# Performance work log

Measured on AMD Instinct MI355X. Metric: run time of the kernel, lower is better.

The kernel has to match this reference:

```python
import jax, jax.numpy as jnp
import numpy as np

B, A, EMBED, HIDDEN, PROJ = 256, 16, 1024, 1024, 256


def setup_inputs() -> dict:
    key = jax.random.key(0)
    k0, k1, k2 = jax.random.split(key, 3)
    return {
        "agent_embeddings": jax.random.normal(k0, (B, A, EMBED), dtype=jnp.float32),
        "w1": jax.random.normal(k1, (EMBED, HIDDEN), dtype=jnp.float32) * (1.0 / np.sqrt(EMBED)),
        "b1": jnp.zeros((HIDDEN,), dtype=jnp.float32),
        "w2": jax.random.normal(k2, (HIDDEN, PROJ), dtype=jnp.float32) * (1.0 / np.sqrt(HIDDEN)),
        "b2": jnp.zeros((PROJ,), dtype=jnp.float32),
        "log_scale": jnp.asarray(0.0, dtype=jnp.float32),  # log(init_logit_scale=1.0)
        "logit_bias": jnp.asarray(0.0, dtype=jnp.float32),
    }


def reference(agent_embeddings, w1, b1, w2, b2, log_scale, logit_bias):
    b, a, d = agent_embeddings.shape
    n = b * a
    x = agent_embeddings.reshape(n, d)
    # MLP projector: Linear -> GELU (exact, torch default) -> [dropout=identity at eval] -> Linear
    h = jax.nn.gelu(x @ w1 + b1, approximate=False)
    p = h @ w2 + b2  # [N, proj_dim]
    z = p / jnp.linalg.norm(p, axis=-1, keepdims=True)
    # cosine similarity logits, scaled + biased
    logits = (z @ z.T) * jnp.exp(log_scale) + logit_bias  # [N, N]
    # block-diagonal labels: 1 iff same batch element
    ids = jnp.arange(n) // a
    m1 = jnp.where(ids[:, None] == ids[None, :], 1.0, -1.0)  # 2*labels - 1
    loglik = jax.nn.log_sigmoid(m1 * logits)
    loss = jnp.mean(-jnp.sum(loglik, axis=-1))
    embeddings = z.reshape(b, a, -1)
    return embeddings, loss, logits
```

## Files before the change

### kernel.cpp

```cpp
#include <hip/hip_runtime.h>
#include <math.h>


#define NTOK 4096
#define DEMB 1024
#define DHID 1024
#define DPRJ 256

typedef __attribute__((ext_vector_type(8))) short bf16x8;
typedef __attribute__((ext_vector_type(4))) float f32x4;

typedef __attribute__((address_space(3))) void lds_void_t;
typedef __attribute__((address_space(1))) const void gbl_void_t;

static __device__ __forceinline__ void glds16(const void* g, void* l) {
    __builtin_amdgcn_global_load_lds((gbl_void_t*)g, (lds_void_t*)l, 16, 0, 0);
}

static __device__ __forceinline__ void split2(float v, ushort* h, ushort* l) {
    const uint u = __float_as_uint(v);
    *h = (ushort)(u >> 16);
    const float r = v - __uint_as_float(u & 0xffff0000u);
    *l = (ushort)(__float_as_uint(r) >> 16);
}
static __device__ __forceinline__ float gelu_fast(float v) {
    const float x  = v * 0.70710678118654752440f;
    const float ax = fabsf(x);
    const float t  = 1.0f / (1.0f + 0.3275911f * ax);
    const float poly = t * (0.254829592f + t * (-0.284496736f + t * (1.421413741f
                     + t * (-1.453152027f + t * 1.061405429f))));
    const float erf_ax = 1.0f - poly * __expf(-ax * ax);
    return 0.5f * v * (1.0f + copysignf(erf_ax, x));
}
static __device__ __forceinline__ float log_sigmoid_fast(float x) {
    return fminf(x, 0.0f) - __logf(1.0f + __expf(-fabsf(x)));
}

__global__ __launch_bounds__(256)
void k_cvt_T(const float* __restrict__ W, ushort* __restrict__ WtH,
             ushort* __restrict__ WtL, int K, int N)
{
    __shared__ float tile[32][33];
    const int tn0 = blockIdx.x * 32;
    const int tk0 = blockIdx.y * 32;
    const int tr = threadIdx.x >> 5;
    const int tc = threadIdx.x & 31;
#pragma unroll
    for (int p = 0; p < 4; ++p)
        tile[tr + 8 * p][tc] = W[(size_t)(tk0 + tr + 8 * p) * N + tn0 + tc];
    __syncthreads();
#pragma unroll
    for (int p = 0; p < 4; ++p) {
        const int n = tr + 8 * p;
        ushort h, l;
        split2(tile[tc][n], &h, &l);
        WtH[(size_t)(tn0 + n) * K + tk0 + tc] = h;
        WtL[(size_t)(tn0 + n) * K + tk0 + tc] = l;
    }
}

#define G1_BUF 12288
__global__ __launch_bounds__(256, 3)
void k_gemm1(const float* __restrict__ X,
             const ushort* __restrict__ W1tH, const ushort* __restrict__ W1tL,
             const float* __restrict__ B1,
             ushort* __restrict__ Hh, ushort* __restrict__ Hl)
{
    __shared__ __align__(16) ushort sm[2 * G1_BUF];
    const int t = threadIdx.x, lane = t & 63, w = t >> 6;
    const int wr = w >> 1, wc = w & 1;
    const int bm = blockIdx.x * 128, bn = blockIdx.y * 64;
    const int kb = lane >> 4, lr = lane & 15;

    const int ar = t & 63;
    const float* xp0 = X + (size_t)(bm + ar) * DEMB + w * 8;
    const float* xp1 = xp0 + (size_t)64 * DEMB;
    const ushort* bhs = W1tH + (size_t)(bn + lane) * DEMB + w * 8;
    const ushort* bls = W1tL + (size_t)(bn + lane) * DEMB + w * 8;

    f32x4 acc[4][2];
#pragma unroll
    for (int i = 0; i < 4; ++i)
#pragma unroll
        for (int j = 0; j < 2; ++j) acc[i][j] = (f32x4){0.f, 0.f, 0.f, 0.f};

    {
        const float4 a00 = *(const float4*)(xp0);
        const float4 a01 = *(const float4*)(xp0 + 4);
        const float4 a10 = *(const float4*)(xp1);
        const float4 a11 = *(const float4*)(xp1 + 4);
        glds16(bhs, sm + 8192 + w * 512);
        glds16(bls, sm + 10240 + w * 512);
        const float va[8] = {a00.x, a00.y, a00.z, a00.w, a01.x, a01.y, a01.z, a01.w};
        const float vb[8] = {a10.x, a10.y, a10.z, a10.w, a11.x, a11.y, a11.z, a11.w};
        uint4 h0, l0, h1, l1;
#pragma unroll
        for (int e = 0; e < 8; ++e) {
            split2(va[e], (ushort*)&h0 + e, (ushort*)&l0 + e);
            split2(vb[e], (ushort*)&h1 + e, (ushort*)&l1 + e);
        }
        *(uint4*)(sm + w * 1024 + ar * 8)               = h0;
        *(uint4*)(sm + 4096 + w * 1024 + ar * 8)        = l0;
        *(uint4*)(sm + w * 1024 + (ar + 64) * 8)        = h1;
        *(uint4*)(sm + 4096 + w * 1024 + (ar + 64) * 8) = l1;
        __syncthreads();
    }

    int co = 0;
#pragma unroll 2
    for (int ks = 0; ks < 32; ++ks) {
        float4 a00, a01, a10, a11;
        if (ks < 31) {
            const int kt = (ks + 1) * 32;
            a00 = *(const float4*)(xp0 + kt);
            a01 = *(const float4*)(xp0 + kt + 4);
            a10 = *(const float4*)(xp1 + kt);
            a11 = *(const float4*)(xp1 + kt + 4);
            ushort* nb = sm + (co ^ G1_BUF);
            glds16(bhs + kt, nb + 8192 + w * 512);
            glds16(bls + kt, nb + 10240 + w * 512);
        }
        const ushort* cb = sm + co;
        bf16x8 bh[2], bl[2];
#pragma unroll
        for (int j = 0; j < 2; ++j) {
            const int o = kb * 512 + (wc * 32 + j * 16 + lr) * 8;
            bh[j] = *(const bf16x8*)(cb + 8192 + o);
            bl[j] = *(const bf16x8*)(cb + 10240 + o);
        }
#pragma unroll
        for (int i = 0; i < 4; ++i) {
            const int o = kb * 1024 + (wr * 64 + i * 16 + lr) * 8;
            const bf16x8 ah = *(const bf16x8*)(cb + o);
            const bf16x8 al = *(const bf16x8*)(cb + 4096 + o);
#pragma unroll
            for (int j = 0; j < 2; ++j) {
                acc[i][j] = __builtin_amdgcn_mfma_f32_16x16x32_bf16(ah, bh[j], acc[i][j], 0, 0, 0);
                acc[i][j] = __builtin_amdgcn_mfma_f32_16x16x32_bf16(ah, bl[j], acc[i][j], 0, 0, 0);
                acc[i][j] = __builtin_amdgcn_mfma_f32_16x16x32_bf16(al, bh[j], acc[i][j], 0, 0, 0);
            }
        }
        if (ks < 31) {
            ushort* nb = sm + (co ^ G1_BUF);
            const float va[8] = {a00.x, a00.y, a00.z, a00.w, a01.x, a01.y, a01.z, a01.w};
            const float vb[8] = {a10.x, a10.y, a10.z, a10.w, a11.x, a11.y, a11.z, a11.w};
            uint4 h0, l0, h1, l1;
#pragma unroll
            for (int e = 0; e < 8; ++e) {
                split2(va[e], (ushort*)&h0 + e, (ushort*)&l0 + e);
                split2(vb[e], (ushort*)&h1 + e, (ushort*)&l1 + e);
            }
            *(uint4*)(nb + w * 1024 + ar * 8)               = h0;
            *(uint4*)(nb + 4096 + w * 1024 + ar * 8)        = l0;
            *(uint4*)(nb + w * 1024 + (ar + 64) * 8)        = h1;
            *(uint4*)(nb + 4096 + w * 1024 + (ar + 64) * 8) = l1;
        }
        __syncthreads();
        co ^= G1_BUF;
    }

#pragma unroll
    for (int j = 0; j < 2; ++j) {
        const int col = bn + wc * 32 + j * 16 + lr;
        const float b = B1[col];
#pragma unroll
        for (int i = 0; i < 4; ++i) {
#pragma unroll
            for (int e = 0; e < 4; ++e) {
                const int row = bm + wr * 64 + i * 16 + kb * 4 + e;
                const float g = gelu_fast(acc[i][j][e] + b);
                ushort h, l;
                split2(g, &h, &l);
                Hh[(size_t)row * DHID + col] = h;
                Hl[(size_t)row * DHID + col] = l;
            }
        }
    }
}

#define G2_BUF 12288
__global__ __launch_bounds__(256, 3)
void k_gemm2(const ushort* __restrict__ Hh, const ushort* __restrict__ Hl,
             const ushort* __restrict__ W2tH, const ushort* __restrict__ W2tL,
             float* __restrict__ P)
{
    __shared__ __align__(16) ushort sm[2 * G2_BUF];
    const int t = threadIdx.x, lane = t & 63, w = t >> 6;
    const int wr = w >> 1, wc = w & 1;
    const int bm = blockIdx.x * 128, bn = blockIdx.y * 64;
    const int k0 = blockIdx.z * 512;
    const int kb = lane >> 4, lr = lane & 15;

    const ushort* ah0 = Hh + (size_t)(bm + lane) * DHID + k0 + w * 8;
    const ushort* ah1 = Hh + (size_t)(bm + 64 + lane) * DHID + k0 + w * 8;
    const ushort* al0 = Hl + (size_t)(bm + lane) * DHID + k0 + w * 8;
    const ushort* al1 = Hl + (size_t)(bm + 64 + lane) * DHID + k0 + w * 8;
    const ushort* bhs = W2tH + (size_t)(bn + lane) * DHID + k0 + w * 8;
    const ushort* bls = W2tL + (size_t)(bn + lane) * DHID + k0 + w * 8;

    f32x4 acc[4][2];
#pragma unroll
    for (int i = 0; i < 4; ++i)
#pragma unroll
        for (int j = 0; j < 2; ++j) acc[i][j] = (f32x4){0.f, 0.f, 0.f, 0.f};

#define G2_STAGE(buf, kt)                                   \
    glds16(ah0 + (kt), (buf) + w * 1024);                   \
    glds16(ah1 + (kt), (buf) + w * 1024 + 512);             \
    glds16(al0 + (kt), (buf) + 4096 + w * 1024);            \
    glds16(al1 + (kt), (buf) + 4096 + w * 1024 + 512);      \
    glds16(bhs + (kt), (buf) + 8192 + w * 512);             \
    glds16(bls + (kt), (buf) + 10240 + w * 512);

    { G2_STAGE(sm, 0); __syncthreads(); }

    int co = 0;
#pragma unroll 2
    for (int ks = 0; ks < 16; ++ks) {
        if (ks < 15) {
            ushort* nb = sm + (co ^ G2_BUF);
            const int kt = (ks + 1) * 32;
            G2_STAGE(nb, kt);
        }
        const ushort* cb = sm + co;
        bf16x8 bh[2], bl[2];
#pragma unroll
        for (int j = 0; j < 2; ++j) {
            const int o = kb * 512 + (wc * 32 + j * 16 + lr) * 8;
            bh[j] = *(const bf16x8*)(cb + 8192 + o);
            bl[j] = *(const bf16x8*)(cb + 10240 + o);
        }
#pragma unroll
        for (int i = 0; i < 4; ++i) {
            const int o = kb * 1024 + (wr * 64 + i * 16 + lr) * 8;
            const bf16x8 ah = *(const bf16x8*)(cb + o);
            const bf16x8 al = *(const bf16x8*)(cb + 4096 + o);
#pragma unroll
            for (int j = 0; j < 2; ++j) {
                acc[i][j] = __builtin_amdgcn_mfma_f32_16x16x32_bf16(ah, bh[j], acc[i][j], 0, 0, 0);
                acc[i][j] = __builtin_amdgcn_mfma_f32_16x16x32_bf16(ah, bl[j], acc[i][j], 0, 0, 0);
                acc[i][j] = __builtin_amdgcn_mfma_f32_16x16x32_bf16(al, bh[j], acc[i][j], 0, 0, 0);
            }
        }
        __syncthreads();
        co ^= G2_BUF;
    }

    float* Pz = P + (size_t)blockIdx.z * NTOK * DPRJ;
#pragma unroll
    for (int j = 0; j < 2; ++j) {
        const int col = bn + wc * 32 + j * 16 + lr;
#pragma unroll
        for (int i = 0; i < 4; ++i) {
#pragma unroll
            for (int e = 0; e < 4; ++e) {
                const int row = bm + wr * 64 + i * 16 + kb * 4 + e;
                Pz[(size_t)row * DPRJ + col] = acc[i][j][e];
            }
        }
    }
}

__global__ __launch_bounds__(256)
void k_norm(const float* __restrict__ P, const float* __restrict__ B2,
            float* __restrict__ Zo, ushort* __restrict__ Zbh,
            ushort* __restrict__ Zbl)
{
    const int r = blockIdx.x;
    const int c = threadIdx.x;

    const float v = P[(size_t)r * DPRJ + c]
                  + P[(size_t)NTOK * DPRJ + (size_t)r * DPRJ + c] + B2[c];
    float ss = v * v;
#pragma unroll
    for (int o = 32; o > 0; o >>= 1) ss += __shfl_down(ss, o);
    __shared__ float wsum[4];
    if ((c & 63) == 0) wsum[c >> 6] = ss;
    __syncthreads();
    const float tot = wsum[0] + wsum[1] + wsum[2] + wsum[3];
    const float z = v / sqrtf(tot);
    Zo[(size_t)r * DPRJ + c] = z;
    ushort h, l;
    split2(z, &h, &l);
    Zbh[(size_t)r * DPRJ + c] = h;
    Zbl[(size_t)r * DPRJ + c] = l;
}

__global__ __launch_bounds__(512, 1)
void k_gemm3(const ushort* __restrict__ Zbh, const ushort* __restrict__ Zbl,
             const float* __restrict__ LS, const float* __restrict__ LB,
             float* __restrict__ Lg, float* __restrict__ partial)
{
    __shared__ __align__(16) ushort sm[65536];
    ushort* Ah = sm;
    ushort* Al = sm + 16384;
    ushort* Bh = sm + 32768;
    ushort* Bl = sm + 49152;

    const int t = threadIdx.x, lane = t & 63, w = t >> 6;
    const int wr = w >> 2, wc = w & 3;
    const int bm = blockIdx.x * 128, bn = blockIdx.y * 128;
    const int kb = lane >> 4, lr = lane & 15;

    const int srow0 = w * 16;

    f32x4 acc[4][2];
#pragma unroll
    for (int i = 0; i < 4; ++i)
#pragma unroll
        for (int j = 0; j < 2; ++j) acc[i][j] = (f32x4){0.f, 0.f, 0.f, 0.f};

    float lsum = 0.0f;

#pragma unroll
    for (int ph = 0; ph < 2; ++ph) {
        const int ko = ph * 128;
        if (ph) __syncthreads();

#pragma unroll
        for (int q = 0; q < 4; ++q) {
            const int row = srow0 + q * 4 + (lane >> 4);
            const int gck = (lane & 15) ^ (row & 15);
            const size_t ga = (size_t)(bm + row) * DPRJ + ko + (gck << 3);
            const size_t gb = (size_t)(bn + row) * DPRJ + ko + (gck << 3);
            const int lo = (srow0 + q * 4) * 128;
            glds16(Zbh + ga, Ah + lo);
            glds16(Zbl + ga, Al + lo);
            glds16(Zbh + gb, Bh + lo);
            glds16(Zbl + gb, Bl + lo);
        }
        __syncthreads();

#pragma unroll
        for (int ks = 0; ks < 4; ++ks) {
            const int g = ks * 4 + kb;
            bf16x8 bhf[2], blf[2];
#pragma unroll
            for (int j = 0; j < 2; ++j) {
                const int col = wc * 32 + j * 16 + lr;
                const int o = col * 128 + ((g ^ (col & 15)) << 3);
                bhf[j] = *(const bf16x8*)(Bh + o);
                blf[j] = *(const bf16x8*)(Bl + o);
            }
#pragma unroll
            for (int i = 0; i < 4; ++i) {
                const int row = wr * 64 + i * 16 + lr;
                const int o = row * 128 + ((g ^ (row & 15)) << 3);
                const bf16x8 ah = *(const bf16x8*)(Ah + o);
                const bf16x8 al = *(const bf16x8*)(Al + o);
#pragma unroll
                for (int j = 0; j < 2; ++j) {
                    acc[i][j] = __builtin_amdgcn_mfma_f32_16x16x32_bf16(ah, bhf[j], acc[i][j], 0, 0, 0);
                    acc[i][j] = __builtin_amdgcn_mfma_f32_16x16x32_bf16(ah, blf[j], acc[i][j], 0, 0, 0);
                    acc[i][j] = __builtin_amdgcn_mfma_f32_16x16x32_bf16(al, bhf[j], acc[i][j], 0, 0, 0);
                }
            }
        }
    }

    const float scale = __expf(LS[0]);
    const float lbias = LB[0];

    __syncthreads();
    float* fT = (float*)sm;
#pragma unroll
    for (int j = 0; j < 2; ++j) {
        const int col = bn + wc * 32 + j * 16 + lr;
        const int cid = col >> 4;
#pragma unroll
        for (int i = 0; i < 4; ++i) {
#pragma unroll
            for (int e = 0; e < 4; ++e) {
                const int rloc = wr * 64 + i * 16 + kb * 4 + e;
                const float lg = fmaf(acc[i][j][e], scale, lbias);
                fT[rloc * 132 + (wc * 32 + j * 16 + lr)] = lg;
                const float x = (((bm + rloc) >> 4) == cid) ? lg : -lg;
                lsum += log_sigmoid_fast(x);
            }
        }
    }
    __syncthreads();

#pragma unroll
    for (int q = 0; q < 32; ++q) {
        const int e = q * 512 + t;
        const int row = e >> 7, c = e & 127;
        Lg[(size_t)(bm + row) * NTOK + bn + c] = fT[row * 132 + c];
    }

#pragma unroll
    for (int o = 32; o > 0; o >>= 1) lsum += __shfl_down(lsum, o);
    __shared__ float wsum[8];
    if (lane == 0) wsum[w] = lsum;
    __syncthreads();
    if (t == 0) {
        float s = 0.f;
#pragma unroll
        for (int i = 0; i < 8; ++i) s += wsum[i];
        partial[blockIdx.y * gridDim.x + blockIdx.x] = s;
    }
}

__global__ __launch_bounds__(256)
void k_finalize(const float* __restrict__ partial, float* __restrict__ loss_out)
{
    const int t = threadIdx.x;
    double s = (double)partial[t] + (double)partial[t + 256]
             + (double)partial[t + 512] + (double)partial[t + 768];
#pragma unroll
    for (int o = 32; o > 0; o >>= 1) s += __shfl_down(s, o);
    __shared__ double ws4[4];
    if ((t & 63) == 0) ws4[t >> 6] = s;
    __syncthreads();
    if (t == 0)
        loss_out[0] = (float)(-(ws4[0] + ws4[1] + ws4[2] + ws4[3]) / (double)NTOK);
}

extern "C" void kernel_launch(void* const* d_in, const int* in_sizes, int n_in,
                              void* d_out, int out_size, void* d_ws, size_t ws_size,
                              hipStream_t stream)
{
    const float* X  = (const float*)d_in[0];
    const float* W1 = (const float*)d_in[1];
    const float* B1 = (const float*)d_in[2];
    const float* W2 = (const float*)d_in[3];
    const float* B2 = (const float*)d_in[4];
    const float* LS = (const float*)d_in[5];
    const float* LB = (const float*)d_in[6];

    float* out  = (float*)d_out;
    float* Zo   = out;
    float* loss = out + (size_t)NTOK * DPRJ;
    float* Lg   = loss + 1;

    char* ws = (char*)d_ws;
    ushort* Hh   = (ushort*)(ws);
    ushort* Hl   = (ushort*)(ws + 8388608);
    ushort* W1tH = (ushort*)(ws + 16777216);
    ushort* W1tL = (ushort*)(ws + 18874368);
    float*  P    = (float*) (ws + 16777216);
    ushort* W2tH = (ushort*)(ws + 25165824);
    ushort* W2tL = (ushort*)(ws + 25690112);
    ushort* Zbh  = (ushort*)(ws + 26214400);
    ushort* Zbl  = (ushort*)(ws + 28311552);
    float*  part = (float*) (ws + 30408704);

    k_cvt_T <<<dim3(32, 32),    256, 0, stream>>>(W1, W1tH, W1tL, DEMB, DHID);
    k_cvt_T <<<dim3(8, 32),     256, 0, stream>>>(W2, W2tH, W2tL, DHID, DPRJ);
    k_gemm1 <<<dim3(32, 16),    256, 0, stream>>>(X, W1tH, W1tL, B1, Hh, Hl);
    k_gemm2 <<<dim3(32, 4, 2),  256, 0, stream>>>(Hh, Hl, W2tH, W2tL, P);
    k_norm  <<<dim3(4096),      256, 0, stream>>>(P, B2, Zo, Zbh, Zbl);
    k_gemm3 <<<dim3(32, 32),    512, 0, stream>>>(Zbh, Zbl, LS, LB, Lg, part);
    k_finalize<<<1, 256, 0, stream>>>(part, loss);
}
```

Before: 223.1 us.

## Pre-split X to bf16 hi/lo and restructure GEMM1/GEMM2 with swizzled LDS tiles

Adds a separate kernel that splits X into bf16 hi/lo halves, processing it in two 2048-row halves so the staging buffer fits the workspace. GEMM1 and GEMM2 then load A and B directly into XOR-swizzled LDS with global_load_lds, using 512-thread blocks with 8 waves and 128-wide K phases. This replaces the earlier in-loop float-to-bf16 conversion and double-buffered 32-wide K steps. The new phases are single-buffered with a barrier before each load, so load and compute no longer overlap within a block. The extra conversion launches add memory traffic and launch overhead.

```diff
diff --git a/kernel.cpp b/kernel.cpp
--- a/kernel.cpp
+++ b/kernel.cpp
@@ -59,204 +59,174 @@
     }
 }
 
-#define G1_BUF 12288
-__global__ __launch_bounds__(256, 3)
-void k_gemm1(const float* __restrict__ X,
+__global__ __launch_bounds__(256)
+void k_cvt_X(const float* __restrict__ X, ushort* __restrict__ Xh,
+             ushort* __restrict__ Xl)
+{
+    const size_t idx = ((size_t)blockIdx.x * 256 + threadIdx.x) * 8;
+    const float4 v0 = *(const float4*)(X + idx);
+    const float4 v1 = *(const float4*)(X + idx + 4);
+    const float vv[8] = {v0.x, v0.y, v0.z, v0.w, v1.x, v1.y, v1.z, v1.w};
+    uint4 hv, lv;
+#pragma unroll
+    for (int e = 0; e < 8; ++e)
+        split2(vv[e], (ushort*)&hv + e, (ushort*)&lv + e);
+    *(uint4*)(Xh + idx) = hv;
+    *(uint4*)(Xl + idx) = lv;
+}
+
+__global__ __launch_bounds__(512, 1)
+void k_gemm1(const ushort* __restrict__ Xh, const ushort* __restrict__ Xl,
              const ushort* __restrict__ W1tH, const ushort* __restrict__ W1tL,
-             const float* __restrict__ B1,
+             const float* __restrict__ B1, int bm0,
              ushort* __restrict__ Hh, ushort* __restrict__ Hl)
 {
-    __shared__ __align__(16) ushort sm[2 * G1_BUF];
+    __shared__ __align__(16) ushort sm[49152];
+    ushort* Ah = sm;
+    ushort* Al = sm + 16384;
+    ushort* Bh = sm + 32768;
+    ushort* Bl = sm + 40960;
+
     const int t = threadIdx.x, lane = t & 63, w = t >> 6;
-    const int wr = w >> 1, wc = w & 1;
-    const int bm = blockIdx.x * 128, bn = blockIdx.y * 64;
+    const int wr = w >> 2, wc = w & 3;
+    const int bmr = blockIdx.x * 128;
+    const int bn  = blockIdx.y * 64;
     const int kb = lane >> 4, lr = lane & 15;
 
-    const int ar = t & 63;
-    const float* xp0 = X + (size_t)(bm + ar) * DEMB + w * 8;
-    const float* xp1 = xp0 + (size_t)64 * DEMB;
-    const ushort* bhs = W1tH + (size_t)(bn + lane) * DEMB + w * 8;
-    const ushort* bls = W1tL + (size_t)(bn + lane) * DEMB + w * 8;
-
-    f32x4 acc[4][2];
-#pragma unroll
-    for (int i = 0; i < 4; ++i)
-#pragma unroll
-        for (int j = 0; j < 2; ++j) acc[i][j] = (f32x4){0.f, 0.f, 0.f, 0.f};
-
-    {
-        const float4 a00 = *(const float4*)(xp0);
-        const float4 a01 = *(const float4*)(xp0 + 4);
-        const float4 a10 = *(const float4*)(xp1);
-        const float4 a11 = *(const float4*)(xp1 + 4);
-        glds16(bhs, sm + 8192 + w * 512);
-        glds16(bls, sm + 10240 + w * 512);
-        const float va[8] = {a00.x, a00.y, a00.z, a00.w, a01.x, a01.y, a01.z, a01.w};
-        const float vb[8] = {a10.x, a10.y, a10.z, a10.w, a11.x, a11.y, a11.z, a11.w};
-        uint4 h0, l0, h1, l1;
-#pragma unroll
-        for (int e = 0; e < 8; ++e) {
-            split2(va[e], (ushort*)&h0 + e, (ushort*)&l0 + e);
-            split2(vb[e], (ushort*)&h1 + e, (ushort*)&l1 + e);
-        }
-        *(uint4*)(sm + w * 1024 + ar * 8)               = h0;
-        *(uint4*)(sm + 4096 + w * 1024 + ar * 8)        = l0;
-        *(uint4*)(sm + w * 1024 + (ar + 64) * 8)        = h1;
-        *(uint4*)(sm + 4096 + w * 1024 + (ar + 64) * 8) = l1;
+    f32x4 acc[4];
+#pragma unroll
+    for (int i = 0; i < 4; ++i) acc[i] = (f32x4){0.f, 0.f, 0.f, 0.f};
+
+    for (int ph = 0; ph < 8; ++ph) {
+        const int ko = ph * 128;
+        if (ph) __syncthreads();
+#pragma unroll
+        for (int q = 0; q < 4; ++q) {
+            const int row = w * 16 + q * 4 + (lane >> 4);
+            const int gck = (lane & 15) ^ (row & 15);
+            const size_t ga = (size_t)(bmr + row) * DEMB + ko + (gck << 3);
+            const int lo = (w * 16 + q * 4) * 128;
+            glds16(Xh + ga, Ah + lo);
+            glds16(Xl + ga, Al + lo);
+        }
+#pragma unroll
+        for (int q = 0; q < 2; ++q) {
+            const int row = w * 8 + q * 4 + (lane >> 4);
+            const int gck = (lane & 15) ^ (row & 15);
+            const size_t gb = (size_t)(bn + row) * DEMB + ko + (gck << 3);
+            const int lo = (w * 8 + q * 4) * 128;
+            glds16(W1tH + gb, Bh + lo);
+            glds16(W1tL + gb, Bl + lo);
+        }
         __syncthreads();
-    }
-
-    int co = 0;
-#pragma unroll 2
-    for (int ks = 0; ks < 32; ++ks) {
-        float4 a00, a01, a10, a11;
-        if (ks < 31) {
-            const int kt = (ks + 1) * 32;
-            a00 = *(const float4*)(xp0 + kt);
-            a01 = *(const float4*)(xp0 + kt + 4);
-            a10 = *(const float4*)(xp1 + kt);
-            a11 = *(const float4*)(xp1 + kt + 4);
-            ushort* nb = sm + (co ^ G1_BUF);
-            glds16(bhs + kt, nb + 8192 + w * 512);
-            glds16(bls + kt, nb + 10240 + w * 512);
-        }
-        const ushort* cb = sm + co;
-        bf16x8 bh[2], bl[2];
-#pragma unroll
-        for (int j = 0; j < 2; ++j) {
-            const int o = kb * 512 + (wc * 32 + j * 16 + lr) * 8;
-            bh[j] = *(const bf16x8*)(cb + 8192 + o);
-            bl[j] = *(const bf16x8*)(cb + 10240 + o);
-        }
-#pragma unroll
-        for (int i = 0; i < 4; ++i) {
-            const int o = kb * 1024 + (wr * 64 + i * 16 + lr) * 8;
-            const bf16x8 ah = *(const bf16x8*)(cb + o);
-            const bf16x8 al = *(const bf16x8*)(cb + 4096 + o);
-#pragma unroll
-            for (int j = 0; j < 2; ++j) {
-                acc[i][j] = __builtin_amdgcn_mfma_f32_16x16x32_bf16(ah, bh[j], acc[i][j], 0, 0, 0);
-                acc[i][j] = __builtin_amdgcn_mfma_f32_16x16x32_bf16(ah, bl[j], acc[i][j], 0, 0, 0);
-                acc[i][j] = __builtin_amdgcn_mfma_f32_16x16x32_bf16(al, bh[j], acc[i][j], 0, 0, 0);
+#pragma unroll
+        for (int ks = 0; ks < 4; ++ks) {
+            const int g = ks * 4 + kb;
+            const int colL = wc * 16 + lr;
+            const int ob = colL * 128 + ((g ^ (colL & 15)) << 3);
+            const bf16x8 bh = *(const bf16x8*)(Bh + ob);
+            const bf16x8 bl = *(const bf16x8*)(Bl + ob);
+#pragma unroll
+            for (int i = 0; i < 4; ++i) {
+                const int rowL = wr * 64 + i * 16 + lr;
+                const int oa = rowL * 128 + ((g ^ (rowL & 15)) << 3);
+                const bf16x8 ah = *(const bf16x8*)(Ah + oa);
+                const bf16x8 al = *(const bf16x8*)(Al + oa);
+                acc[i] = __builtin_amdgcn_mfma_f32_16x16x32_bf16(ah, bh, acc[i], 0, 0, 0);
+                acc[i] = __builtin_amdgcn_mfma_f32_16x16x32_bf16(ah, bl, acc[i], 0, 0, 0);
+                acc[i] = __builtin_amdgcn_mfma_f32_16x16x32_bf16(al, bh, acc[i], 0, 0, 0);
             }
         }
-        if (ks < 31) {
-            ushort* nb = sm + (co ^ G1_BUF);
-            const float va[8] = {a00.x, a00.y, a00.z, a00.w, a01.x, a01.y, a01.z, a01.w};
-            const float vb[8] = {a10.x, a10.y, a10.z, a10.w, a11.x, a11.y, a11.z, a11.w};
-            uint4 h0, l0, h1, l1;
-#pragma unroll
-            for (int e = 0; e < 8; ++e) {
-                split2(va[e], (ushort*)&h0 + e, (ushort*)&l0 + e);
-                split2(vb[e], (ushort*)&h1 + e, (ushort*)&l1 + e);
-            }
-            *(uint4*)(nb + w * 1024 + ar * 8)               = h0;
-            *(uint4*)(nb + 4096 + w * 1024 + ar * 8)        = l0;
-            *(uint4*)(nb + w * 1024 + (ar + 64) * 8)        = h1;
-            *(uint4*)(nb + 4096 + w * 1024 + (ar + 64) * 8) = l1;
-        }
-        __syncthreads();
-        co ^= G1_BUF;
-    }
-
-#pragma unroll
-    for (int j = 0; j < 2; ++j) {
-        const int col = bn + wc * 32 + j * 16 + lr;
-        const float b = B1[col];
-#pragma unroll
-        for (int i = 0; i < 4; ++i) {
-#pragma unroll
-            for (int e = 0; e < 4; ++e) {
-                const int row = bm + wr * 64 + i * 16 + kb * 4 + e;
-                const float g = gelu_fast(acc[i][j][e] + b);
-                ushort h, l;
-                split2(g, &h, &l);
-                Hh[(size_t)row * DHID + col] = h;
-                Hl[(size_t)row * DHID + col] = l;
-            }
-        }
-    }
-}
-
-#define G2_BUF 12288
-__global__ __launch_bounds__(256, 3)
+    }
+
+    const int col = bn + wc * 16 + lr;
+    const float b = B1[col];
+#pragma unroll
+    for (int i = 0; i < 4; ++i) {
+#pragma unroll
+        for (int e = 0; e < 4; ++e) {
+            const int row = bm0 + bmr + wr * 64 + i * 16 + kb * 4 + e;
+            const float g = gelu_fast(acc[i][e] + b);
+            ushort h, l;
+            split2(g, &h, &l);
+            Hh[(size_t)row * DHID + col] = h;
+            Hl[(size_t)row * DHID + col] = l;
+        }
+    }
+}
+
+__global__ __launch_bounds__(512, 1)
 void k_gemm2(const ushort* __restrict__ Hh, const ushort* __restrict__ Hl,
              const ushort* __restrict__ W2tH, const ushort* __restrict__ W2tL,
              float* __restrict__ P)
 {
-    __shared__ __align__(16) ushort sm[2 * G2_BUF];
+    __shared__ __align__(16) ushort sm[49152];
+    ushort* Ah = sm;
+    ushort* Al = sm + 16384;
+    ushort* Bh = sm + 32768;
+    ushort* Bl = sm + 40960;
+
     const int t = threadIdx.x, lane = t & 63, w = t >> 6;
-    const int wr = w >> 1, wc = w & 1;
-    const int bm = blockIdx.x * 128, bn = blockIdx.y * 64;
-    const int k0 = blockIdx.z * 512;
+    const int wr = w >> 2, wc = w & 3;
+    const int bmr = blockIdx.x * 128;
+    const int bn  = blockIdx.y * 64;
+    const int k0  = blockIdx.z * 512;
     const int kb = lane >> 4, lr = lane & 15;
 
-    const ushort* ah0 = Hh + (size_t)(bm + lane) * DHID + k0 + w * 8;
-    const ushort* ah1 = Hh + (size_t)(bm + 64 + lane) * DHID + k0 + w * 8;
-    const ushort* al0 = Hl + (size_t)(bm + lane) * DHID + k0 + w * 8;
-    const ushort* al1 = Hl + (size_t)(bm + 64 + lane) * DHID + k0 + w * 8;
-    const ushort* bhs = W2tH + (size_t)(bn + lane) * DHID + k0 + w * 8;
-    const ushort* bls = W2tL + (size_t)(bn + lane) * DHID + k0 + w * 8;
-
-    f32x4 acc[4][2];
-#pragma unroll
-    for (int i = 0; i < 4; ++i)
-#pragma unroll
-        for (int j = 0; j < 2; ++j) acc[i][j] = (f32x4){0.f, 0.f, 0.f, 0.f};
-
-#define G2_STAGE(buf, kt)                                   \
-    glds16(ah0 + (kt), (buf) + w * 1024);                   \
-    glds16(ah1 + (kt), (buf) + w * 1024 + 512);             \
-    glds16(al0 + (kt), (buf) + 4096 + w * 1024);            \
-    glds16(al1 + (kt), (buf) + 4096 + w * 1024 + 512);      \
-    glds16(bhs + (kt), (buf) + 8192 + w * 512);             \
-    glds16(bls + (kt), (buf) + 10240 + w * 512);
-
-    { G2_STAGE(sm, 0); __syncthreads(); }
-
-    int co = 0;
-#pragma unroll 2
-    for (int ks = 0; ks < 16; ++ks) {
-        if (ks < 15) {
-            ushort* nb = sm + (co ^ G2_BUF);
-            const int kt = (ks + 1) * 32;
-            G2_STAGE(nb, kt);
-        }
-        const ushort* cb = sm + co;
-        bf16x8 bh[2], bl[2];
-#pragma unroll
-        for (int j = 0; j < 2; ++j) {
-            const int o = kb * 512 + (wc * 32 + j * 16 + lr) * 8;
-            bh[j] = *(const bf16x8*)(cb + 8192 + o);
-            bl[j] = *(const bf16x8*)(cb + 10240 + o);
-        }
-#pragma unroll
-        for (int i = 0; i < 4; ++i) {
-            const int o = kb * 1024 + (wr * 64 + i * 16 + lr) * 8;
-            const bf16x8 ah = *(const bf16x8*)(cb + o);
-            const bf16x8 al = *(const bf16x8*)(cb + 4096 + o);
-#pragma unroll
-            for (int j = 0; j < 2; ++j) {
-                acc[i][j] = __builtin_amdgcn_mfma_f32_16x16x32_bf16(ah, bh[j], acc[i][j], 0, 0, 0);
-                acc[i][j] = __builtin_amdgcn_mfma_f32_16x16x32_bf16(ah, bl[j], acc[i][j], 0, 0, 0);
-                acc[i][j] = __builtin_amdgcn_mfma_f32_16x16x32_bf16(al, bh[j], acc[i][j], 0, 0, 0);
+    f32x4 acc[4];
+#pragma unroll
+    for (int i = 0; i < 4; ++i) acc[i] = (f32x4){0.f, 0.f, 0.f, 0.f};
+
+    for (int ph = 0; ph < 4; ++ph) {
+        const int ko = k0 + ph * 128;
+        if (ph) __syncthreads();
+#pragma unroll
+        for (int q = 0; q < 4; ++q) {
+            const int row = w * 16 + q * 4 + (lane >> 4);
+            const int gck = (lane & 15) ^ (row & 15);
+            const size_t ga = (size_t)(bmr + row) * DHID + ko + (gck << 3);
+            const int lo = (w * 16 + q * 4) * 128;
+            glds16(Hh + ga, Ah + lo);
+            glds16(Hl + ga, Al + lo);
+        }
+#pragma unroll
+        for (int q = 0; q < 2; ++q) {
+            const int row = w * 8 + q * 4 + (lane >> 4);
+            const int gck = (lane & 15) ^ (row & 15);
+            const size_t gb = (size_t)(bn + row) * DHID + ko + (gck << 3);
+            const int lo = (w * 8 + q * 4) * 128;
+            glds16(W2tH + gb, Bh + lo);
+            glds16(W2tL + gb, Bl + lo);
+        }
+        __syncthreads();
+#pragma unroll
+        for (int ks = 0; ks < 4; ++ks) {
+            const int g = ks * 4 + kb;
+            const int colL = wc * 16 + lr;
+            const int ob = colL * 128 + ((g ^ (colL & 15)) << 3);
+            const bf16x8 bh = *(const bf16x8*)(Bh + ob);
+            const bf16x8 bl = *(const bf16x8*)(Bl + ob);
+#pragma unroll
+            for (int i = 0; i < 4; ++i) {
+                const int rowL = wr * 64 + i * 16 + lr;
+                const int oa = rowL * 128 + ((g ^ (rowL & 15)) << 3);
+                const bf16x8 ah = *(const bf16x8*)(Ah + oa);
+                const bf16x8 al = *(const bf16x8*)(Al + oa);
+                acc[i] = __builtin_amdgcn_mfma_f32_16x16x32_bf16(ah, bh, acc[i], 0, 0, 0);
+                acc[i] = __builtin_amdgcn_mfma_f32_16x16x32_bf16(ah, bl, acc[i], 0, 0, 0);
+                acc[i] = __builtin_amdgcn_mfma_f32_16x16x32_bf16(al, bh, acc[i], 0, 0, 0);
             }
         }
-        __syncthreads();
-        co ^= G2_BUF;
     }
 
     float* Pz = P + (size_t)blockIdx.z * NTOK * DPRJ;
-#pragma unroll
-    for (int j = 0; j < 2; ++j) {
-        const int col = bn + wc * 32 + j * 16 + lr;
-#pragma unroll
-        for (int i = 0; i < 4; ++i) {
-#pragma unroll
-            for (int e = 0; e < 4; ++e) {
-                const int row = bm + wr * 64 + i * 16 + kb * 4 + e;
-                Pz[(size_t)row * DPRJ + col] = acc[i][j][e];
-            }
+    const int col = bn + wc * 16 + lr;
+#pragma unroll
+    for (int i = 0; i < 4; ++i) {
+#pragma unroll
+        for (int e = 0; e < 4; ++e) {
+            const int row = bmr + wr * 64 + i * 16 + kb * 4 + e;
+            Pz[(size_t)row * DPRJ + col] = acc[i][e];
         }
     }
 }
@@ -301,7 +271,6 @@
     const int wr = w >> 2, wc = w & 3;
     const int bm = blockIdx.x * 128, bn = blockIdx.y * 128;
     const int kb = lane >> 4, lr = lane & 15;
-
     const int srow0 = w * 16;
 
     f32x4 acc[4][2];
@@ -316,7 +285,6 @@
     for (int ph = 0; ph < 2; ++ph) {
         const int ko = ph * 128;
         if (ph) __syncthreads();
-
 #pragma unroll
         for (int q = 0; q < 4; ++q) {
             const int row = srow0 + q * 4 + (lane >> 4);
@@ -330,7 +298,6 @@
             glds16(Zbl + gb, Bl + lo);
         }
         __syncthreads();
-
 #pragma unroll
         for (int ks = 0; ks < 4; ++ks) {
             const int g = ks * 4 + kb;
@@ -436,20 +403,26 @@
     char* ws = (char*)d_ws;
     ushort* Hh   = (ushort*)(ws);
     ushort* Hl   = (ushort*)(ws + 8388608);
-    ushort* W1tH = (ushort*)(ws + 16777216);
-    ushort* W1tL = (ushort*)(ws + 18874368);
+    ushort* Xsh  = (ushort*)(ws + 16777216);
+    ushort* Xsl  = (ushort*)(ws + 20971520);
     float*  P    = (float*) (ws + 16777216);
-    ushort* W2tH = (ushort*)(ws + 25165824);
-    ushort* W2tL = (ushort*)(ws + 25690112);
-    ushort* Zbh  = (ushort*)(ws + 26214400);
-    ushort* Zbl  = (ushort*)(ws + 28311552);
+    ushort* W1tH = (ushort*)(ws + 25165824);
+    ushort* W1tL = (ushort*)(ws + 27262976);
+    ushort* Zbh  = (ushort*)(ws + 25165824);
+    ushort* Zbl  = (ushort*)(ws + 27262976);
+    ushort* W2tH = (ushort*)(ws + 29360128);
+    ushort* W2tL = (ushort*)(ws + 29884416);
     float*  part = (float*) (ws + 30408704);
 
-    k_cvt_T <<<dim3(32, 32),    256, 0, stream>>>(W1, W1tH, W1tL, DEMB, DHID);
-    k_cvt_T <<<dim3(8, 32),     256, 0, stream>>>(W2, W2tH, W2tL, DHID, DPRJ);
-    k_gemm1 <<<dim3(32, 16),    256, 0, stream>>>(X, W1tH, W1tL, B1, Hh, Hl);
-    k_gemm2 <<<dim3(32, 4, 2),  256, 0, stream>>>(Hh, Hl, W2tH, W2tL, P);
-    k_norm  <<<dim3(4096),      256, 0, stream>>>(P, B2, Zo, Zbh, Zbl);
-    k_gemm3 <<<dim3(32, 32),    512, 0, stream>>>(Zbh, Zbl, LS, LB, Lg, part);
+    k_cvt_T <<<dim3(32, 32),   256, 0, stream>>>(W1, W1tH, W1tL, DEMB, DHID);
+    k_cvt_T <<<dim3(8, 32),    256, 0, stream>>>(W2, W2tH, W2tL, DHID, DPRJ);
+    k_cvt_X <<<dim3(1024),     256, 0, stream>>>(X, Xsh, Xsl);
+    k_gemm1 <<<dim3(16, 16),   512, 0, stream>>>(Xsh, Xsl, W1tH, W1tL, B1, 0, Hh, Hl);
+    k_cvt_X <<<dim3(1024),     256, 0, stream>>>(X + (size_t)2048 * DEMB, Xsh, Xsl);
+    k_gemm1 <<<dim3(16, 16),   512, 0, stream>>>(Xsh, Xsl, W1tH, W1tL, B1, 2048, Hh, Hl);
+
+    k_gemm2 <<<dim3(32, 4, 2), 512, 0, stream>>>(Hh, Hl, W2tH, W2tL, P);
+    k_norm  <<<dim3(4096),     256, 0, stream>>>(P, B2, Zo, Zbh, Zbl);
+    k_gemm3 <<<dim3(32, 32),   512, 0, stream>>>(Zbh, Zbl, LS, LB, Lg, part);
     k_finalize<<<1, 256, 0, stream>>>(part, loss);
 }
```

After: 208.1 us. 6.7% less time.
